# Kernel optimization log

Measured on AMD Instinct MI355X. Metric: run time of the kernel, lower is better.

## Reference

```python
import jax, jax.numpy as jnp
import numpy as np

TOPK_RATIO = 0.2
DICE_WEIGHT = 0.5
SHAPE = (2, 1, 128, 192, 192)


def setup_inputs() -> dict:
    key = jax.random.key(0)
    k1, k2 = jax.random.split(key)
    logits = jax.random.normal(k1, SHAPE, dtype=jnp.float32)
    targets = jax.random.uniform(k2, SHAPE, dtype=jnp.float32)
    return {"logits": logits, "targets": targets}


def _bce_with_logits(x, t):
    # stable: max(x,0) - x*t + log(1+exp(-|x|))
    return jnp.maximum(x, 0.0) - x * t + jnp.log1p(jnp.exp(-jnp.abs(x)))


def reference(logits, targets):
    # --- TopK BCE ---
    flat_loss = _bce_with_logits(logits, targets).reshape(-1)
    n = flat_loss.shape[0]
    k_samples = max(1, int(n * TOPK_RATIO))
    topk_losses, _ = jax.lax.top_k(flat_loss, k_samples)
    bce = jnp.mean(topk_losses)

    # --- Soft Dice ---
    p = jax.nn.sigmoid(logits).reshape(-1)
    t = targets.reshape(-1)
    intersection = jnp.sum(p * t)
    union = jnp.sum(p) + jnp.sum(t)
    dice = (2.0 * intersection + 1e-06) / (union + 1e-06)
    dice_loss = 1.0 - dice

    return bce + DICE_WEIGHT * dice_loss
```

## Files before the change

### kernel.cpp

```cpp
#include <hip/hip_runtime.h>
#include <math.h>
#include <limits.h>

#define NB1 2048
#define OFF1 6656
#define NB2 4096
#define NREP 4
#define GRID_MAIN 2048

__device__ unsigned g_H1[NB1];
__device__ unsigned g_hist2[NREP * NB2];
__device__ float    g_band[2];
__device__ unsigned g_done1 = 0;

__device__ __forceinline__ void elem_f(float x, float t, float& l, float& p) {
    float e = __expf(-fabsf(x));
    l = fmaxf(x, 0.f) - x * t + __logf(1.f + e);
    float r = __builtin_amdgcn_rcpf(1.f + e);
    p = (x >= 0.f) ? r : e * r;
}

__device__ __forceinline__ int coarse_bin(float l) {
    int b = (int)(__float_as_uint(l) >> 17) - OFF1;
    return min(max(b, 0), NB1 - 1);
}

__global__ __launch_bounds__(256) void sample_band_kernel(
    const float4* __restrict__ x4, const float4* __restrict__ t4,
    int n4, long long ks, long long M)
{
    __shared__ unsigned lh[NB1];
    __shared__ int is_last;
    for (int i = threadIdx.x; i < NB1; i += 256) lh[i] = 0u;
    __syncthreads();

    int nth = gridDim.x * 256;
    int tid = blockIdx.x * 256 + threadIdx.x;
    int S4 = n4 >> 4;
    int i0 = tid, i1 = tid + nth;

    float4 xa, ta, xb, tb;
    bool v0 = i0 < S4, v1 = i1 < S4;
    if (v0) {
        int f4 = ((i0 >> 6) << 10) + (i0 & 63);
        xa = x4[f4]; ta = t4[f4];
    }
    if (v1) {
        int f4 = ((i1 >> 6) << 10) + (i1 & 63);
        xb = x4[f4]; tb = t4[f4];
    }
    if (v0) {
        float xs[4] = {xa.x, xa.y, xa.z, xa.w};
        float ts[4] = {ta.x, ta.y, ta.z, ta.w};
        #pragma unroll
        for (int c = 0; c < 4; ++c) {
            float l, p; elem_f(xs[c], ts[c], l, p);
            atomicAdd(&lh[coarse_bin(l)], 1u);
        }
    }
    if (v1) {
        float xs[4] = {xb.x, xb.y, xb.z, xb.w};
        float ts[4] = {tb.x, tb.y, tb.z, tb.w};
        #pragma unroll
        for (int c = 0; c < 4; ++c) {
            float l, p; elem_f(xs[c], ts[c], l, p);
            atomicAdd(&lh[coarse_bin(l)], 1u);
        }
    }
    __syncthreads();
    for (int i = threadIdx.x; i < NB1; i += 256) {
        unsigned c = lh[i];
        if (c) atomicAdd(&g_H1[i], c);
    }
    __syncthreads();

    if (threadIdx.x == 0) {
        __threadfence();
        is_last = (atomicAdd(&g_done1, 1u) == (unsigned)(gridDim.x - 1));
    }
    __syncthreads();
    if (!is_last) return;
    __threadfence();

    const uint4* hv = (const uint4*)g_H1;
    uint4* lv = (uint4*)lh;
    for (int i = threadIdx.x; i < NB1 / 4; i += 256) lv[i] = hv[i];
    __syncthreads();
    for (int i = threadIdx.x; i < NB1; i += 256) g_H1[i] = 0u;
    if (threadIdx.x == 0) g_done1 = 0u;

    if (threadIdx.x < 64) {
        int lane = threadIdx.x;
        int base = lane << 5;
        unsigned long long chunk = 0;
        for (int j = 0; j < 32; ++j) chunk += lh[base + j];
        unsigned long long s = chunk;
        #pragma unroll
        for (int off = 1; off < 64; off <<= 1) {
            unsigned long long v = __shfl_down(s, off);
            if (lane + off < 64) s += v;
        }
        unsigned long long above = s - chunk;

        int my_bhi = INT_MAX, my_blo = -1;
        unsigned long long c = above;
        for (int j = 31; j >= 0; --j) {
            unsigned h = lh[base + j];
            if ((long long)(c + h) < ks - M) my_bhi = base + j;
            if ((long long)c > ks + M && my_blo < 0) my_blo = base + j;
            c += h;
        }
        #pragma unroll
        for (int off = 32; off; off >>= 1) {
            int a = __shfl_down(my_bhi, off); my_bhi = min(my_bhi, a);
            int b = __shfl_down(my_blo, off); my_blo = max(my_blo, b);
        }
        if (lane == 0) {
            int bhi = (my_bhi == INT_MAX) ? (NB1 - 1) : my_bhi;
            int blo = my_blo;
            float vhi = __uint_as_float((unsigned)(bhi + OFF1) << 17);
            float vlo = (blo < 0) ? 0.f
                                  : __uint_as_float((unsigned)(blo + 1 + OFF1) << 17);
            if (!(vlo < vhi)) vlo = 0.f;
            g_band[0] = vlo;
            g_band[1] = vhi;
        }
    }
}

__global__ __launch_bounds__(256) void main_kernel(
    const float4* __restrict__ x4, const float4* __restrict__ t4,
    float* __restrict__ q0, float* __restrict__ q1,
    float* __restrict__ q2, float* __restrict__ q3, unsigned* __restrict__ qc,
    const float* __restrict__ xg, const float* __restrict__ tg,
    int n, int n4)
{
    __shared__ unsigned lhist[NB2];
    for (int i = threadIdx.x; i < NB2; i += 256) lhist[i] = 0u;
    __syncthreads();

    float vlo = g_band[0], vhi = g_band[1];
    float scale = (float)NB2 / (vhi - vlo);

    int per = (n4 + GRID_MAIN - 1) / GRID_MAIN;
    int base = blockIdx.x * per;
    int end = min(base + per, n4);

    float sp = 0.f, spt = 0.f, st = 0.f, sgt = 0.f;
    unsigned cnt = 0;

    for (int idx = base + threadIdx.x; idx < end; idx += 256) {
        float4 xv = x4[idx], tv = t4[idx];
        float xs[4] = {xv.x, xv.y, xv.z, xv.w};
        float ts[4] = {tv.x, tv.y, tv.z, tv.w};
        #pragma unroll
        for (int c = 0; c < 4; ++c) {
            float l, p;
            elem_f(xs[c], ts[c], l, p);
            sp += p; spt += p * ts[c]; st += ts[c];
            if (l >= vhi) { cnt++; sgt += l; }
            else if (l >= vlo) {
                int b = min((int)((l - vlo) * scale), NB2 - 1);
                atomicAdd(&lhist[b], 1u);
            }
        }
    }

    int tail0 = n4 << 2;
    if (blockIdx.x == 0 && threadIdx.x < (n - tail0)) {
        float x = xg[tail0 + threadIdx.x], t = tg[tail0 + threadIdx.x];
        float l, p;
        elem_f(x, t, l, p);
        sp += p; spt += p * t; st += t;
        if (l >= vhi) { cnt++; sgt += l; }
        else if (l >= vlo) {
            int b = min((int)((l - vlo) * scale), NB2 - 1);
            atomicAdd(&lhist[b], 1u);
        }
    }

    __syncthreads();
    {
        unsigned* dst = &g_hist2[(blockIdx.x & (NREP - 1)) * NB2];
        for (int i = threadIdx.x; i < NB2; i += 256) {
            unsigned c = lhist[i];
            if (c) atomicAdd(&dst[i], c);
        }
    }

    #pragma unroll
    for (int off = 32; off; off >>= 1) {
        sp  += __shfl_down(sp,  off);
        spt += __shfl_down(spt, off);
        st  += __shfl_down(st,  off);
        sgt += __shfl_down(sgt, off);
        cnt += __shfl_down(cnt, off);
    }
    __shared__ float    rs[4][4];
    __shared__ unsigned rc[4];
    int w = threadIdx.x >> 6;
    if ((threadIdx.x & 63) == 0) {
        rs[w][0] = sp; rs[w][1] = spt; rs[w][2] = st; rs[w][3] = sgt; rc[w] = cnt;
    }
    __syncthreads();
    if (threadIdx.x == 0) {
        float a0 = 0, a1 = 0, a2 = 0, a3 = 0;
        unsigned c = 0;
        #pragma unroll
        for (int i = 0; i < 4; ++i) {
            a0 += rs[i][0]; a1 += rs[i][1]; a2 += rs[i][2]; a3 += rs[i][3]; c += rc[i];
        }
        q0[blockIdx.x] = a0; q1[blockIdx.x] = a1; q2[blockIdx.x] = a2;
        q3[blockIdx.x] = a3; qc[blockIdx.x] = c;
    }
}

__global__ __launch_bounds__(1024) void final_kernel(
    const float* __restrict__ q0, const float* __restrict__ q1,
    const float* __restrict__ q2, const float* __restrict__ q3,
    const unsigned* __restrict__ qc, int nblocks,
    float* __restrict__ out, long long k)
{
    __shared__ unsigned lh[NB2];
    __shared__ double red[16][5];
    __shared__ double fin[5];

    for (int i = threadIdx.x; i < NB2; i += 1024) {
        unsigned s = 0;
        #pragma unroll
        for (int r = 0; r < NREP; ++r) {
            s += g_hist2[r * NB2 + i];
            g_hist2[r * NB2 + i] = 0u;
        }
        lh[i] = s;
    }

    double a0 = 0, a1 = 0, a2 = 0, a3 = 0, a4 = 0;
    for (int i = threadIdx.x; i < nblocks; i += 1024) {
        a0 += (double)q0[i]; a1 += (double)q1[i]; a2 += (double)q2[i];
        a3 += (double)q3[i]; a4 += (double)qc[i];
    }
    #pragma unroll
    for (int off = 32; off; off >>= 1) {
        a0 += __shfl_down(a0, off); a1 += __shfl_down(a1, off);
        a2 += __shfl_down(a2, off); a3 += __shfl_down(a3, off);
        a4 += __shfl_down(a4, off);
    }
    int w = threadIdx.x >> 6;
    if ((threadIdx.x & 63) == 0) {
        red[w][0] = a0; red[w][1] = a1; red[w][2] = a2; red[w][3] = a3; red[w][4] = a4;
    }
    __syncthreads();
    if (threadIdx.x == 0) {
        double f0 = 0, f1 = 0, f2 = 0, f3 = 0, f4 = 0;
        for (int i = 0; i < 16; ++i) {
            f0 += red[i][0]; f1 += red[i][1]; f2 += red[i][2];
            f3 += red[i][3]; f4 += red[i][4];
        }
        fin[0] = f0; fin[1] = f1; fin[2] = f2; fin[3] = f3; fin[4] = f4;
    }
    __syncthreads();
    if (threadIdx.x >= 64) return;

    int lane = threadIdx.x;
    double SP = fin[0], SPT = fin[1], ST = fin[2], SGT = fin[3];
    long long CNT = (long long)fin[4];

    double vlo = (double)g_band[0], vhi = (double)g_band[1];
    double binw = (vhi - vlo) / NB2;
    long long k2 = k - CNT;

    int base = lane << 6;
    unsigned long long cchunk = 0;
    double wchunk = 0.0;
    for (int j = 0; j < 64; ++j) {
        unsigned h = lh[base + j];
        cchunk += h;
        wchunk += (double)h * (vlo + (base + j + 0.5) * binw);
    }
    unsigned long long cs = cchunk;
    double wsum = wchunk;
    #pragma unroll
    for (int off = 1; off < 64; off <<= 1) {
        unsigned long long cv = __shfl_down(cs, off);
        double wv = __shfl_down(wsum, off);
        if (lane + off < 64) { cs += cv; wsum += wv; }
    }
    unsigned long long total = __shfl(cs, 0);
    double wtotal = __shfl(wsum, 0);

    double I = SPT, U = SP + ST;
    double dice_part = 0.5 * (1.0 - (2.0 * I + 1e-6) / (U + 1e-6));

    if (k2 <= 0) {
        if (lane == 0) out[0] = (float)(SGT / (double)k + dice_part);
        return;
    }
    if ((unsigned long long)k2 > total) {
        if (lane == 0) {
            double sum_top = SGT + wtotal + (double)(k2 - (long long)total) * vlo;
            out[0] = (float)(sum_top / (double)k + dice_part);
        }
        return;
    }
    unsigned long long c = cs - cchunk;
    double wacc = wsum - wchunk;
    for (int j = 63; j >= 0; --j) {
        unsigned h = lh[base + j];
        double val = vlo + (base + j + 0.5) * binw;
        if (c < (unsigned long long)k2 && (unsigned long long)k2 <= c + h) {
            double sum_top = SGT + wacc + (double)((long long)k2 - (long long)c) * val;
            out[0] = (float)(sum_top / (double)k + dice_part);
        }
        c += h;
        wacc += (double)h * val;
    }
}

extern "C" void kernel_launch(void* const* d_in, const int* in_sizes, int n_in,
                              void* d_out, int out_size, void* d_ws, size_t ws_size,
                              hipStream_t stream)
{
    const float* x = (const float*)d_in[0];
    const float* t = (const float*)d_in[1];
    float* out = (float*)d_out;
    int n = in_sizes[0];
    int n4 = n >> 2;
    long long k = (long long)((double)n * 0.2);
    if (k < 1) k = 1;

    long long S = (long long)(n4 >> 4) * 4;
    long long ks = (S > 0) ? (long long)((double)k * (double)S / (double)n) : 0;
    long long M = 4096;

    int S4 = n4 >> 4;
    int sgrid = (S4 + 511) / 512;
    if (sgrid < 1) sgrid = 1;

    unsigned char* ws = (unsigned char*)d_ws;
    size_t pstride = (((size_t)GRID_MAIN * 4) + 255) & ~(size_t)255;
    float*    q0 = (float*)(ws);
    float*    q1 = (float*)(ws + pstride);
    float*    q2 = (float*)(ws + 2 * pstride);
    float*    q3 = (float*)(ws + 3 * pstride);
    unsigned* qc = (unsigned*)(ws + 4 * pstride);

    sample_band_kernel<<<sgrid, 256, 0, stream>>>((const float4*)x, (const float4*)t,
                                                  n4, ks, M);
    main_kernel<<<GRID_MAIN, 256, 0, stream>>>((const float4*)x, (const float4*)t,
                                               q0, q1, q2, q3, qc, x, t, n, n4);
    final_kernel<<<1, 1024, 0, stream>>>(q0, q1, q2, q3, qc, GRID_MAIN, out, k);
}
```

Baseline: 132.5 us.

## Fuse sampling and main passes into one persistent kernel with grid barrier

```diff
diff --git a/kernel.cpp b/kernel.cpp
--- a/kernel.cpp
+++ b/kernel.cpp
@@ -6,12 +6,12 @@
 #define OFF1 6656
 #define NB2 4096
 #define NREP 4
-#define GRID_MAIN 2048
 
 __device__ unsigned g_H1[NB1];
 __device__ unsigned g_hist2[NREP * NB2];
 __device__ float    g_band[2];
-__device__ unsigned g_done1 = 0;
+__device__ unsigned g_bar = 0;
+__device__ unsigned g_rel = 0;
 
 __device__ __forceinline__ void elem_f(float x, float t, float& l, float& p) {
     float e = __expf(-fabsf(x));
@@ -25,75 +25,68 @@
     return min(max(b, 0), NB1 - 1);
 }
 
-__global__ __launch_bounds__(256) void sample_band_kernel(
+__global__ __launch_bounds__(256) void fused_kernel(
     const float4* __restrict__ x4, const float4* __restrict__ t4,
-    int n4, long long ks, long long M)
+    float* __restrict__ q0, float* __restrict__ q1,
+    float* __restrict__ q2, float* __restrict__ q3, unsigned* __restrict__ qc,
+    const float* __restrict__ xg, const float* __restrict__ tg,
+    int n, int n4, int per, long long ks, long long M)
 {
-    __shared__ unsigned lh[NB1];
-    __shared__ int is_last;
-    for (int i = threadIdx.x; i < NB1; i += 256) lh[i] = 0u;
-    __syncthreads();
-
-    int nth = gridDim.x * 256;
-    int tid = blockIdx.x * 256 + threadIdx.x;
-    int S4 = n4 >> 4;
-    int i0 = tid, i1 = tid + nth;
-
-    float4 xa, ta, xb, tb;
-    bool v0 = i0 < S4, v1 = i1 < S4;
-    if (v0) {
-        int f4 = ((i0 >> 6) << 10) + (i0 & 63);
-        xa = x4[f4]; ta = t4[f4];
-    }
-    if (v1) {
-        int f4 = ((i1 >> 6) << 10) + (i1 & 63);
-        xb = x4[f4]; tb = t4[f4];
-    }
-    if (v0) {
+    __shared__ unsigned lhist[NB2];
+    __shared__ float    sband[2];
+    __shared__ float    rs[4][4];
+    __shared__ unsigned rc[4];
+
+    int tid = threadIdx.x;
+    long long base = (long long)blockIdx.x * per;
+    int bbase = (base < n4) ? (int)base : n4;
+    int bend  = min(bbase + per, n4);
+    int avail = bend - bbase;
+
+    for (int i = tid; i < NB1; i += 256) lhist[i] = 0u;
+    __syncthreads();
+
+    int scnt = avail >> 4;
+    for (int i = tid; i < scnt; i += 256) {
+        float4 xa = x4[bbase + i], ta = t4[bbase + i];
         float xs[4] = {xa.x, xa.y, xa.z, xa.w};
         float ts[4] = {ta.x, ta.y, ta.z, ta.w};
         #pragma unroll
         for (int c = 0; c < 4; ++c) {
             float l, p; elem_f(xs[c], ts[c], l, p);
-            atomicAdd(&lh[coarse_bin(l)], 1u);
-        }
-    }
-    if (v1) {
-        float xs[4] = {xb.x, xb.y, xb.z, xb.w};
-        float ts[4] = {tb.x, tb.y, tb.z, tb.w};
-        #pragma unroll
-        for (int c = 0; c < 4; ++c) {
-            float l, p; elem_f(xs[c], ts[c], l, p);
-            atomicAdd(&lh[coarse_bin(l)], 1u);
-        }
-    }
-    __syncthreads();
-    for (int i = threadIdx.x; i < NB1; i += 256) {
-        unsigned c = lh[i];
+            atomicAdd(&lhist[coarse_bin(l)], 1u);
+        }
+    }
+    __syncthreads();
+    for (int i = tid; i < NB1; i += 256) {
+        unsigned c = lhist[i];
         if (c) atomicAdd(&g_H1[i], c);
     }
     __syncthreads();
 
-    if (threadIdx.x == 0) {
+    if (tid == 0) {
         __threadfence();
-        is_last = (atomicAdd(&g_done1, 1u) == (unsigned)(gridDim.x - 1));
-    }
-    __syncthreads();
-    if (!is_last) return;
-    __threadfence();
-
-    const uint4* hv = (const uint4*)g_H1;
-    uint4* lv = (uint4*)lh;
-    for (int i = threadIdx.x; i < NB1 / 4; i += 256) lv[i] = hv[i];
-    __syncthreads();
-    for (int i = threadIdx.x; i < NB1; i += 256) g_H1[i] = 0u;
-    if (threadIdx.x == 0) g_done1 = 0u;
-
-    if (threadIdx.x < 64) {
-        int lane = threadIdx.x;
-        int base = lane << 5;
+        unsigned a = atomicAdd(&g_bar, 1u);
+        if (a == gridDim.x - 1) {
+            __hip_atomic_store(&g_rel, 1u, __ATOMIC_RELEASE,
+                               __HIP_MEMORY_SCOPE_AGENT);
+        } else {
+            while (__hip_atomic_load(&g_rel, __ATOMIC_ACQUIRE,
+                                     __HIP_MEMORY_SCOPE_AGENT) == 0u)
+                __builtin_amdgcn_s_sleep(8);
+        }
+        __threadfence();
+    }
+    __syncthreads();
+
+    for (int i = tid; i < NB1; i += 256) lhist[i] = g_H1[i];
+    __syncthreads();
+
+    if (tid < 64) {
+        int lane = tid;
+        int cb = lane << 5;
         unsigned long long chunk = 0;
-        for (int j = 0; j < 32; ++j) chunk += lh[base + j];
+        for (int j = 0; j < 32; ++j) chunk += lhist[cb + j];
         unsigned long long s = chunk;
         #pragma unroll
         for (int off = 1; off < 64; off <<= 1) {
@@ -105,9 +98,9 @@
         int my_bhi = INT_MAX, my_blo = -1;
         unsigned long long c = above;
         for (int j = 31; j >= 0; --j) {
-            unsigned h = lh[base + j];
-            if ((long long)(c + h) < ks - M) my_bhi = base + j;
-            if ((long long)c > ks + M && my_blo < 0) my_blo = base + j;
+            unsigned h = lhist[cb + j];
+            if ((long long)(c + h) < ks - M) my_bhi = cb + j;
+            if ((long long)c > ks + M && my_blo < 0) my_blo = cb + j;
             c += h;
         }
         #pragma unroll
@@ -122,34 +115,22 @@
             float vlo = (blo < 0) ? 0.f
                                   : __uint_as_float((unsigned)(blo + 1 + OFF1) << 17);
             if (!(vlo < vhi)) vlo = 0.f;
-            g_band[0] = vlo;
-            g_band[1] = vhi;
-        }
-    }
-}
-
-__global__ __launch_bounds__(256) void main_kernel(
-    const float4* __restrict__ x4, const float4* __restrict__ t4,
-    float* __restrict__ q0, float* __restrict__ q1,
-    float* __restrict__ q2, float* __restrict__ q3, unsigned* __restrict__ qc,
-    const float* __restrict__ xg, const float* __restrict__ tg,
-    int n, int n4)
-{
-    __shared__ unsigned lhist[NB2];
-    for (int i = threadIdx.x; i < NB2; i += 256) lhist[i] = 0u;
-    __syncthreads();
-
-    float vlo = g_band[0], vhi = g_band[1];
+            sband[0] = vlo;
+            sband[1] = vhi;
+            if (blockIdx.x == 0) { g_band[0] = vlo; g_band[1] = vhi; }
+        }
+    }
+    __syncthreads();
+    float vlo = sband[0], vhi = sband[1];
     float scale = (float)NB2 / (vhi - vlo);
 
-    int per = (n4 + GRID_MAIN - 1) / GRID_MAIN;
-    int base = blockIdx.x * per;
-    int end = min(base + per, n4);
+    for (int i = tid; i < NB2; i += 256) lhist[i] = 0u;
+    __syncthreads();
 
     float sp = 0.f, spt = 0.f, st = 0.f, sgt = 0.f;
     unsigned cnt = 0;
 
-    for (int idx = base + threadIdx.x; idx < end; idx += 256) {
+    for (int idx = bbase + tid; idx < bend; idx += 256) {
         float4 xv = x4[idx], tv = t4[idx];
         float xs[4] = {xv.x, xv.y, xv.z, xv.w};
         float ts[4] = {tv.x, tv.y, tv.z, tv.w};
@@ -167,8 +148,8 @@
     }
 
     int tail0 = n4 << 2;
-    if (blockIdx.x == 0 && threadIdx.x < (n - tail0)) {
-        float x = xg[tail0 + threadIdx.x], t = tg[tail0 + threadIdx.x];
+    if (blockIdx.x == 0 && tid < (n - tail0)) {
+        float x = xg[tail0 + tid], t = tg[tail0 + tid];
         float l, p;
         elem_f(x, t, l, p);
         sp += p; spt += p * t; st += t;
@@ -182,7 +163,7 @@
     __syncthreads();
     {
         unsigned* dst = &g_hist2[(blockIdx.x & (NREP - 1)) * NB2];
-        for (int i = threadIdx.x; i < NB2; i += 256) {
+        for (int i = tid; i < NB2; i += 256) {
             unsigned c = lhist[i];
             if (c) atomicAdd(&dst[i], c);
         }
@@ -196,14 +177,12 @@
         sgt += __shfl_down(sgt, off);
         cnt += __shfl_down(cnt, off);
     }
-    __shared__ float    rs[4][4];
-    __shared__ unsigned rc[4];
-    int w = threadIdx.x >> 6;
-    if ((threadIdx.x & 63) == 0) {
+    int w = tid >> 6;
+    if ((tid & 63) == 0) {
         rs[w][0] = sp; rs[w][1] = spt; rs[w][2] = st; rs[w][3] = sgt; rc[w] = cnt;
     }
     __syncthreads();
-    if (threadIdx.x == 0) {
+    if (tid == 0) {
         float a0 = 0, a1 = 0, a2 = 0, a3 = 0;
         unsigned c = 0;
         #pragma unroll
@@ -234,6 +213,8 @@
         }
         lh[i] = s;
     }
+    for (int i = threadIdx.x; i < NB1; i += 1024) g_H1[i] = 0u;
+    if (threadIdx.x == 0) { g_bar = 0u; g_rel = 0u; }
 
     double a0 = 0, a1 = 0, a2 = 0, a3 = 0, a4 = 0;
     for (int i = threadIdx.x; i < nblocks; i += 1024) {
@@ -329,25 +310,45 @@
     long long k = (long long)((double)n * 0.2);
     if (k < 1) k = 1;
 
-    long long S = (long long)(n4 >> 4) * 4;
+    static int s_grid = 0;
+    if (s_grid == 0) {
+        int dev = 0; hipGetDevice(&dev);
+        int ncu = 0;
+        hipDeviceGetAttribute(&ncu, hipDeviceAttributeMultiprocessorCount, dev);
+        int nb = 0;
+        hipOccupancyMaxActiveBlocksPerMultiprocessor(
+            &nb, reinterpret_cast<const void*>(fused_kernel), 256, 0);
+        if (ncu <= 0) ncu = 256;
+        if (nb < 1) nb = 1;
+        long long g = (long long)nb * ncu;
+        if (g > 4096) g = 4096;
+        s_grid = (int)g;
+    }
+    int grid = s_grid;
+    int per = (n4 + grid - 1) / grid;
+    if (per < 1) per = 1;
+
+    long long Sf4 = 0;
+    for (int b = 0; b < grid; ++b) {
+        long long bs = (long long)b * per;
+        if (bs >= n4) break;
+        long long avail = n4 - bs; if (avail > per) avail = per;
+        Sf4 += (avail >> 4);
+    }
+    long long S = Sf4 * 4;
     long long ks = (S > 0) ? (long long)((double)k * (double)S / (double)n) : 0;
     long long M = 4096;
 
-    int S4 = n4 >> 4;
-    int sgrid = (S4 + 511) / 512;
-    if (sgrid < 1) sgrid = 1;
-
     unsigned char* ws = (unsigned char*)d_ws;
-    size_t pstride = (((size_t)GRID_MAIN * 4) + 255) & ~(size_t)255;
+    size_t pstride = (((size_t)grid * 4) + 255) & ~(size_t)255;
     float*    q0 = (float*)(ws);
     float*    q1 = (float*)(ws + pstride);
     float*    q2 = (float*)(ws + 2 * pstride);
     float*    q3 = (float*)(ws + 3 * pstride);
     unsigned* qc = (unsigned*)(ws + 4 * pstride);
 
-    sample_band_kernel<<<sgrid, 256, 0, stream>>>((const float4*)x, (const float4*)t,
-                                                  n4, ks, M);
-    main_kernel<<<GRID_MAIN, 256, 0, stream>>>((const float4*)x, (const float4*)t,
-                                               q0, q1, q2, q3, qc, x, t, n, n4);
-    final_kernel<<<1, 1024, 0, stream>>>(q0, q1, q2, q3, qc, GRID_MAIN, out, k);
-}
+    fused_kernel<<<grid, 256, 0, stream>>>((const float4*)x, (const float4*)t,
+                                           q0, q1, q2, q3, qc, x, t,
+                                           n, n4, per, ks, M);
+    final_kernel<<<1, 1024, 0, stream>>>(q0, q1, q2, q3, qc, grid, out, k);
+}
```

After: 241.6 us. 82.3% more time.
